# Performance work log

Hardware: AMD Instinct MI355X
Metric: run time of the kernel (lower is better)

## Reference

```python
import jax, jax.numpy as jnp
import numpy as np

HIDDEN = 4096
N_HEADS = 32
N_KV = 8
HEAD_DIM = 128
ROPE_THETA = 10000.0
B, S = 2, 2048


def _rope_neox(x, cos, sin):
    # x: [B,S,H,D]; cos/sin: [B,S,1,D/2]
    half = x.shape[-1] // 2
    x1, x2 = x[..., :half], x[..., half:]
    return jnp.concatenate([x1 * cos - x2 * sin, x2 * cos + x1 * sin], axis=-1)


def setup_inputs() -> dict:
    key = jax.random.key(0)
    k1, k2, k3 = jax.random.split(key, 3)
    hidden_states = jax.random.normal(k1, (B, S, HIDDEN), dtype=jnp.float32)
    positions = jnp.arange(B * S, dtype=jnp.int32).reshape(B, S)
    q_size = N_HEADS * HEAD_DIM
    kv_size = N_KV * HEAD_DIM
    w_qkv = jax.random.normal(k2, (HIDDEN, q_size + 2 * kv_size), dtype=jnp.float32) * (HIDDEN ** -0.5)
    w_o = jax.random.normal(k3, (q_size, HIDDEN), dtype=jnp.float32) * (q_size ** -0.5)
    return {"hidden_states": hidden_states, "positions": positions, "w_qkv": w_qkv, "w_o": w_o}


def reference(hidden_states, positions, w_qkv, w_o):
    q_size = N_HEADS * HEAD_DIM
    kv_size = N_KV * HEAD_DIM
    b, s, _ = hidden_states.shape

    qkv = hidden_states @ w_qkv  # [B,S,q+2kv]
    q = qkv[..., :q_size].reshape(b, s, N_HEADS, HEAD_DIM)
    k = qkv[..., q_size:q_size + kv_size].reshape(b, s, N_KV, HEAD_DIM)
    v = qkv[..., q_size + kv_size:].reshape(b, s, N_KV, HEAD_DIM)

    # RoPE (neox style, full rotary dim)
    inv_freq = 1.0 / (ROPE_THETA ** (jnp.arange(0, HEAD_DIM, 2, dtype=jnp.float32) / HEAD_DIM))
    ang = positions.astype(jnp.float32)[..., None] * inv_freq  # [B,S,D/2]
    cos = jnp.cos(ang)[:, :, None, :]
    sin = jnp.sin(ang)[:, :, None, :]
    q = _rope_neox(q, cos, sin)
    k = _rope_neox(k, cos, sin)

    # GQA: expand kv heads to match q heads
    rep = N_HEADS // N_KV
    k = jnp.repeat(k, rep, axis=2)  # [B,S,H,D]
    v = jnp.repeat(v, rep, axis=2)

    scale = HEAD_DIM ** -0.5
    scores = jnp.einsum('bqhd,bkhd->bhqk', q, k) * scale  # [B,H,S,S]
    causal = jnp.tril(jnp.ones((s, s), dtype=bool))
    scores = jnp.where(causal[None, None], scores, jnp.finfo(scores.dtype).min)
    probs = jax.nn.softmax(scores, axis=-1)
    attn = jnp.einsum('bhqk,bkhd->bqhd', probs, v).reshape(b, s, q_size)
    return attn @ w_o
```

## Files before the change

### kernel.cpp

```cpp
#include <hip/hip_runtime.h>
#include <hip/hip_bf16.h>
#include <stdint.h>
#include <stddef.h>

typedef unsigned short u16;
typedef __bf16 bf16x8 __attribute__((ext_vector_type(8)));
typedef float f32x4 __attribute__((ext_vector_type(4)));
typedef float f32x16 __attribute__((ext_vector_type(16)));
typedef unsigned u32x2 __attribute__((ext_vector_type(2)));

#define NH 32
#define NKV 8
#define HD 128
#define QKV_N 6144
#define SEQ 2048

__device__ __forceinline__ u16 f2b(float x) {
  union { float f; unsigned u; } v; v.f = x;
  unsigned r = v.u + 0x7FFF + ((v.u >> 16) & 1);
  return (u16)(r >> 16);
}
__device__ __forceinline__ float b2f(u16 b) {
  union { float f; unsigned u; } v; v.u = ((unsigned)b) << 16;
  return v.f;
}
__device__ __forceinline__ void gload16(const void* g, void* l) {
  __builtin_amdgcn_global_load_lds((const __attribute__((address_space(1))) unsigned int*)g,
                                   (__attribute__((address_space(3))) unsigned int*)l, 16, 0, 0);
}
template <int N>
__device__ __forceinline__ void vmwait() {
  asm volatile("s_waitcnt vmcnt(%0)" ::"n"(N) : "memory");
}
__device__ __forceinline__ unsigned pk(float lo, float hi) {
  union { __bf16 h[2]; unsigned w; } u;
  u.h[0] = (__bf16)lo; u.h[1] = (__bf16)hi;
  return u.w;
}
__device__ __forceinline__ void plswap(unsigned& a, unsigned& b) {
  u32x2 r = __builtin_amdgcn_permlane32_swap(a, b, false, false);
  a = r.x; b = r.y;
}
__device__ __forceinline__ float pl_partner_max(float x) {
  unsigned u = __float_as_uint(x);
  u32x2 r = __builtin_amdgcn_permlane32_swap(u, u, false, false);
  return fmaxf(__uint_as_float(r.x), __uint_as_float(r.y));
}
__device__ __forceinline__ float pl_partner_sum(float x) {
  unsigned u = __float_as_uint(x);
  u32x2 r = __builtin_amdgcn_permlane32_swap(u, u, false, false);
  return __uint_as_float(r.x) + __uint_as_float(r.y);
}

__global__ void cast_f32_bf16(const float* __restrict__ in, u16* __restrict__ out, int n) {
  int i = (blockIdx.x * blockDim.x + threadIdx.x) * 4;
  if (i >= n) return;
  float4 v = *(const float4*)&in[i];
  ushort4 o;
  o.x = f2b(v.x); o.y = f2b(v.y); o.z = f2b(v.z); o.w = f2b(v.w);
  *(ushort4*)&out[i] = o;
}

__global__ void cast_transpose(const float* __restrict__ in, u16* __restrict__ out, int K, int N) {
  __shared__ float t[32][33];
  int n0 = blockIdx.x * 32, k0 = blockIdx.y * 32;
  int tx = threadIdx.x, ty = threadIdx.y;
#pragma unroll
  for (int i = 0; i < 4; ++i)
    t[ty + i * 8][tx] = in[(size_t)(k0 + ty + i * 8) * N + n0 + tx];
  __syncthreads();
#pragma unroll
  for (int i = 0; i < 4; ++i)
    out[(size_t)(n0 + ty + i * 8) * K + k0 + tx] = f2b(t[tx][ty + i * 8]);
}

__device__ __forceinline__ void storeC(float* C, size_t i, float v) { C[i] = v; }
__device__ __forceinline__ void storeC(u16* C, size_t i, float v) { C[i] = f2b(v); }

#define MFMA16(q, A0, A1, B0, B1)                                                              \
  {                                                                                            \
    _Pragma("unroll") for (int mi = 0; mi < 4; ++mi)                                           \
      _Pragma("unroll") for (int ni = 0; ni < 2; ++ni)                                         \
        acc[q][mi][ni] = __builtin_amdgcn_mfma_f32_16x16x32_bf16(A0[mi], B0[ni], acc[q][mi][ni], 0, 0, 0); \
    _Pragma("unroll") for (int mi = 0; mi < 4; ++mi)                                           \
      _Pragma("unroll") for (int ni = 0; ni < 2; ++ni)                                         \
        acc[q][mi][ni] = __builtin_amdgcn_mfma_f32_16x16x32_bf16(A1[mi], B1[ni], acc[q][mi][ni], 0, 0, 0); \
  }

#define KT256(NOFF, SGHI, SGLO, HASV0, HASV1, VM1)                                             \
  {                                                                                            \
    bf16x8 a0[4], a1[4], bl0[2], bl1[2], bh0[2], bh1[2];                                       \
    _Pragma("unroll") for (int mi = 0; mi < 4; ++mi) {                                         \
      a0[mi] = *(const bf16x8*)(rA0 + (NOFF) + mi * 1024);                                     \
      a1[mi] = *(const bf16x8*)(rA1 + (NOFF) + mi * 1024);                                     \
    }                                                                                          \
    _Pragma("unroll") for (int ni = 0; ni < 2; ++ni) {                                         \
      bl0[ni] = *(const bf16x8*)(rB0 + (NOFF) + ni * 1024);                                    \
      bl1[ni] = *(const bf16x8*)(rB1 + (NOFF) + ni * 1024);                                    \
      bh0[ni] = *(const bf16x8*)(rB0 + (NOFF) + 8192 + ni * 1024);                             \
      bh1[ni] = *(const bf16x8*)(rB1 + (NOFF) + 8192 + ni * 1024);                             \
    }                                                                                          \
    if (SGHI) {                                                                                \
      gload16(pAhi0, dAhi0 + ((NOFF) ^ 16384)); gload16(pAhi1, dAhi1 + ((NOFF) ^ 16384));      \
      pAhi0 += 64; pAhi1 += 64;                                                                \
      gload16(pBlo0, dBlo0 + ((NOFF) ^ 16384)); gload16(pBlo1, dBlo1 + ((NOFF) ^ 16384));      \
      gload16(pBhi0, dBhi0 + ((NOFF) ^ 16384)); gload16(pBhi1, dBhi1 + ((NOFF) ^ 16384));      \
      pBlo0 += 64; pBlo1 += 64; pBhi0 += 64; pBhi1 += 64;                                      \
    }                                                                                          \
    __builtin_amdgcn_s_barrier();                                                              \
    __builtin_amdgcn_s_setprio(1);                                                             \
    MFMA16(0, a0, a1, bl0, bl1)                                                                \
    MFMA16(1, a0, a1, bh0, bh1)                                                                \
    __builtin_amdgcn_s_setprio(0);                                                             \
    __builtin_amdgcn_sched_barrier(0);                                                         \
    if (HASV0) vmwait<8>();                                                                    \
    __builtin_amdgcn_s_barrier();                                                              \
    _Pragma("unroll") for (int mi = 0; mi < 4; ++mi) {                                         \
      a0[mi] = *(const bf16x8*)(rA0 + (NOFF) + 8192 + mi * 1024);                              \
      a1[mi] = *(const bf16x8*)(rA1 + (NOFF) + 8192 + mi * 1024);                              \
    }                                                                                          \
    if (SGLO) {                                                                                \
      gload16(pAlo0, dAlo0 + (NOFF)); gload16(pAlo1, dAlo1 + (NOFF));                          \
      pAlo0 += 64; pAlo1 += 64;                                                                \
    }                                                                                          \
    __builtin_amdgcn_s_barrier();                                                              \
    __builtin_amdgcn_s_setprio(1);                                                             \
    MFMA16(2, a0, a1, bl0, bl1)                                                                \
    MFMA16(3, a0, a1, bh0, bh1)                                                                \
    __builtin_amdgcn_s_setprio(0);                                                             \
    __builtin_amdgcn_sched_barrier(0);                                                         \
    if (HASV1) vmwait<VM1>();                                                                  \
    __builtin_amdgcn_s_barrier();                                                              \
  }

template <typename OutT>
__global__ __launch_bounds__(512, 2) void gemm256(const u16* __restrict__ A, const u16* __restrict__ Bt,
                                                  OutT* __restrict__ C, int M, int N, int K) {
  __shared__ __align__(16) u16 sA[2 * 16384];
  __shared__ __align__(16) u16 sB[2 * 16384];
  const int nbx = N >> 8;
  const int nwg = (M >> 8) * nbx;
  const int cpx = nwg >> 3;
  const int wg = ((int)blockIdx.x & 7) * cpx + ((int)blockIdx.x >> 3);
  const int row0 = (wg / nbx) << 8, col0 = (wg % nbx) << 8;
  const int tid = threadIdx.x, w = tid >> 6, lane = tid & 63;
  const int wm = w >> 2, wn = w & 3;
  const int lq = lane & 15, lh = lane >> 4, x7 = lq & 7;
  const int o0 = (lh ^ x7) << 3, o1 = ((4 + lh) ^ x7) << 3;
  const int nt = K >> 6;

  const int rr = tid >> 3;
  const int swz = ((tid & 7) ^ (rr & 7)) << 3;
  const u16* pAlo0 = A + (size_t)(row0 + rr) * K + swz;
  const u16* pAlo1 = A + (size_t)(row0 + 64 + rr) * K + swz;
  const u16* pAhi0 = A + (size_t)(row0 + 128 + rr) * K + swz;
  const u16* pAhi1 = A + (size_t)(row0 + 192 + rr) * K + swz;
  const u16* pBlo0 = Bt + (size_t)(col0 + rr) * K + swz;
  const u16* pBlo1 = Bt + (size_t)(col0 + 64 + rr) * K + swz;
  const u16* pBhi0 = Bt + (size_t)(col0 + 128 + rr) * K + swz;
  const u16* pBhi1 = Bt + (size_t)(col0 + 192 + rr) * K + swz;
  u16* dAlo0 = sA + w * 512;
  u16* dAlo1 = sA + 4096 + w * 512;
  u16* dAhi0 = sA + 8192 + w * 512;
  u16* dAhi1 = sA + 12288 + w * 512;
  u16* dBlo0 = sB + w * 512;
  u16* dBlo1 = sB + 4096 + w * 512;
  u16* dBhi0 = sB + 8192 + w * 512;
  u16* dBhi1 = sB + 12288 + w * 512;
  const u16* rA0 = sA + (wm * 64 + lq) * 64 + o0;
  const u16* rA1 = sA + (wm * 64 + lq) * 64 + o1;
  const u16* rB0 = sB + (wn * 32 + lq) * 64 + o0;
  const u16* rB1 = sB + (wn * 32 + lq) * 64 + o1;

  f32x4 acc[4][4][2] = {};

  gload16(pAlo0, dAlo0); gload16(pAlo1, dAlo1); pAlo0 += 64; pAlo1 += 64;
  gload16(pBlo0, dBlo0); gload16(pBlo1, dBlo1); pBlo0 += 64; pBlo1 += 64;
  gload16(pBhi0, dBhi0); gload16(pBhi1, dBhi1); pBhi0 += 64; pBhi1 += 64;
  gload16(pAhi0, dAhi0); gload16(pAhi1, dAhi1); pAhi0 += 64; pAhi1 += 64;
  gload16(pAlo0, dAlo0 + 16384); gload16(pAlo1, dAlo1 + 16384); pAlo0 += 64; pAlo1 += 64;
  vmwait<4>();
  __builtin_amdgcn_s_barrier();

  for (int t = 0; t < nt - 2; t += 2) {
    KT256(0, 1, 1, 1, 1, 2)
    KT256(16384, 1, 1, 1, 1, 2)
  }
  KT256(0, 1, 0, 1, 1, 0)
  KT256(16384, 0, 0, 0, 0, 0)

#pragma unroll
  for (int q = 0; q < 4; ++q) {
    const int ah = q >> 1, bh2 = q & 1;
#pragma unroll
    for (int mi = 0; mi < 4; ++mi)
#pragma unroll
      for (int ni = 0; ni < 2; ++ni)
#pragma unroll
        for (int j = 0; j < 4; ++j) {
          const int row = row0 + ah * 128 + wm * 64 + mi * 16 + lh * 4 + j;
          const int col = col0 + bh2 * 128 + wn * 32 + ni * 16 + lq;
          storeC(C, (size_t)row * N + col, acc[q][mi][ni][j]);
        }
  }
}

#define MM24(q, A0, A1)                                                                        \
  {                                                                                            \
    _Pragma("unroll") for (int mi = 0; mi < 4; ++mi)                                           \
      _Pragma("unroll") for (int ni = 0; ni < 3; ++ni)                                         \
        acc[q][mi][ni] = __builtin_amdgcn_mfma_f32_16x16x32_bf16(A0[mi], b0[ni], acc[q][mi][ni], 0, 0, 0); \
    _Pragma("unroll") for (int mi = 0; mi < 4; ++mi)                                           \
      _Pragma("unroll") for (int ni = 0; ni < 3; ++ni)                                         \
        acc[q][mi][ni] = __builtin_amdgcn_mfma_f32_16x16x32_bf16(A1[mi], b1[ni], acc[q][mi][ni], 0, 0, 0); \
  }

#define KT192(NA, NB, SGHI, SGLO, HASV0, HASV1, VM1)                                           \
  {                                                                                            \
    bf16x8 a0[4], a1[4], b0[3], b1[3];                                                         \
    _Pragma("unroll") for (int mi = 0; mi < 4; ++mi) {                                         \
      a0[mi] = *(const bf16x8*)(rA0 + (NA) + mi * 1024);                                       \
      a1[mi] = *(const bf16x8*)(rA1 + (NA) + mi * 1024);                                       \
    }                                                                                          \
    _Pragma("unroll") for (int ni = 0; ni < 3; ++ni) {                                         \
      b0[ni] = *(const bf16x8*)(rB0 + (NB) + ni * 1024);                                       \
      b1[ni] = *(const bf16x8*)(rB1 + (NB) + ni * 1024);                                       \
    }                                                                                          \
    if (SGHI) {                                                                                \
      gload16(pA2, dA2 + ((NA) ^ 16384)); gload16(pA3, dA3 + ((NA) ^ 16384));                  \
      pA2 += 64; pA3 += 64;                                                                    \
      gload16(pB0, dB0 + ((NB) ^ 12288)); gload16(pB1, dB1 + ((NB) ^ 12288));                  \
      gload16(pB2, dB2 + ((NB) ^ 12288));                                                      \
      pB0 += 64; pB1 += 64; pB2 += 64;                                                         \
    }                                                                                          \
    __builtin_amdgcn_s_barrier();                                                              \
    __builtin_amdgcn_s_setprio(1);                                                             \
    MM24(0, a0, a1)                                                                            \
    __builtin_amdgcn_s_setprio(0);                                                             \
    __builtin_amdgcn_sched_barrier(0);                                                         \
    if (HASV0) vmwait<7>();                                                                    \
    __builtin_amdgcn_s_barrier();                                                              \
    _Pragma("unroll") for (int mi = 0; mi < 4; ++mi) {                                         \
      a0[mi] = *(const bf16x8*)(rA0 + (NA) + 8192 + mi * 1024);                                \
      a1[mi] = *(const bf16x8*)(rA1 + (NA) + 8192 + mi * 1024);                                \
    }                                                                                          \
    if (SGLO) {                                                                                \
      gload16(pA0, dA0 + (NA)); gload16(pA1, dA1 + (NA));                                      \
      pA0 += 64; pA1 += 64;                                                                    \
    }                                                                                          \
    __builtin_amdgcn_s_barrier();                                                              \
    __builtin_amdgcn_s_setprio(1);                                                             \
    MM24(1, a0, a1)                                                                            \
    __builtin_amdgcn_s_setprio(0);                                                             \
    __builtin_amdgcn_sched_barrier(0);                                                         \
    if (HASV1) vmwait<VM1>();                                                                  \
    __builtin_amdgcn_s_barrier();                                                              \
  }

__global__ __launch_bounds__(512, 2) void gemm192(const u16* __restrict__ A, const u16* __restrict__ Bt,
                                                  u16* __restrict__ C, int M, int N, int K) {
  __shared__ __align__(16) u16 sA[2 * 16384];
  __shared__ __align__(16) u16 sB[2 * 12288];
  const int nbx = N / 192;
  const int nwg = (M >> 8) * nbx;
  const int cpx = nwg >> 3;
  const int wg = ((int)blockIdx.x & 7) * cpx + ((int)blockIdx.x >> 3);
  const int row0 = (wg / nbx) << 8, col0 = (wg % nbx) * 192;
  const int tid = threadIdx.x, w = tid >> 6, lane = tid & 63;
  const int wm = w >> 2, wn = w & 3;
  const int lq = lane & 15, lh = lane >> 4, x7 = lq & 7;
  const int o0 = (lh ^ x7) << 3, o1 = ((4 + lh) ^ x7) << 3;
  const int nt = K >> 6;

  const int rr = tid >> 3;
  const int swz = ((tid & 7) ^ (rr & 7)) << 3;
  const u16* pA0 = A + (size_t)(row0 + rr) * K + swz;
  const u16* pA1 = A + (size_t)(row0 + 64 + rr) * K + swz;
  const u16* pA2 = A + (size_t)(row0 + 128 + rr) * K + swz;
  const u16* pA3 = A + (size_t)(row0 + 192 + rr) * K + swz;
  const u16* pB0 = Bt + (size_t)(col0 + rr) * K + swz;
  const u16* pB1 = Bt + (size_t)(col0 + 64 + rr) * K + swz;
  const u16* pB2 = Bt + (size_t)(col0 + 128 + rr) * K + swz;
  u16* dA0 = sA + w * 512;
  u16* dA1 = sA + 4096 + w * 512;
  u16* dA2 = sA + 8192 + w * 512;
  u16* dA3 = sA + 12288 + w * 512;
  u16* dB0 = sB + w * 512;
  u16* dB1 = sB + 4096 + w * 512;
  u16* dB2 = sB + 8192 + w * 512;
  const u16* rA0 = sA + (wm * 64 + lq) * 64 + o0;
  const u16* rA1 = sA + (wm * 64 + lq) * 64 + o1;
  const u16* rB0 = sB + (wn * 48 + lq) * 64 + o0;
  const u16* rB1 = sB + (wn * 48 + lq) * 64 + o1;

  f32x4 acc[2][4][3] = {};

  gload16(pA0, dA0); gload16(pA1, dA1); pA0 += 64; pA1 += 64;
  gload16(pB0, dB0); gload16(pB1, dB1); gload16(pB2, dB2); pB0 += 64; pB1 += 64; pB2 += 64;
  gload16(pA2, dA2); gload16(pA3, dA3); pA2 += 64; pA3 += 64;
  gload16(pA0, dA0 + 16384); gload16(pA1, dA1 + 16384); pA0 += 64; pA1 += 64;
  vmwait<4>();
  __builtin_amdgcn_s_barrier();

  for (int t = 0; t < nt - 2; t += 2) {
    KT192(0, 0, 1, 1, 1, 1, 2)
    KT192(16384, 12288, 1, 1, 1, 1, 2)
  }
  KT192(0, 0, 1, 0, 1, 1, 0)
  KT192(16384, 12288, 0, 0, 0, 0, 0)

#pragma unroll
  for (int ah = 0; ah < 2; ++ah)
#pragma unroll
    for (int mi = 0; mi < 4; ++mi)
#pragma unroll
      for (int ni = 0; ni < 3; ++ni)
#pragma unroll
        for (int j = 0; j < 4; ++j) {
          const int row = row0 + ah * 128 + wm * 64 + mi * 16 + lh * 4 + j;
          const int col = col0 + wn * 48 + ni * 16 + lq;
          C[(size_t)row * N + col] = f2b(acc[ah][mi][ni][j]);
        }
}

__global__ void rope_kernel(u16* __restrict__ qkv, const int* __restrict__ pos, float qscale) {
  __shared__ float cs[64], sn[64];
  const int row = blockIdx.x;
  const int tid = threadIdx.x;
  if (tid < 64) {
    float p = (float)pos[row];
    float inv = exp2f(-(float)tid * 0.20762050593046f);
    float a = p * inv;
    cs[tid] = cosf(a);
    sn[tid] = sinf(a);
  }
  __syncthreads();
  const size_t base = (size_t)row * QKV_N;
  for (int i = tid; i < 40 * 16; i += 256) {
    const int h = i >> 4, dq = (i & 15) * 4;
    const size_t o = base + h * 128 + dq;
    ushort4 v1 = *(const ushort4*)&qkv[o];
    ushort4 v2 = *(const ushort4*)&qkv[o + 64];
    const float sc = (h < NH) ? qscale : 1.0f;
    ushort4 r1, r2;
    {
      float x1 = b2f(v1.x), x2 = b2f(v2.x), c = cs[dq], s = sn[dq];
      r1.x = f2b((x1 * c - x2 * s) * sc); r2.x = f2b((x2 * c + x1 * s) * sc);
    }
    {
      float x1 = b2f(v1.y), x2 = b2f(v2.y), c = cs[dq + 1], s = sn[dq + 1];
      r1.y = f2b((x1 * c - x2 * s) * sc); r2.y = f2b((x2 * c + x1 * s) * sc);
    }
    {
      float x1 = b2f(v1.z), x2 = b2f(v2.z), c = cs[dq + 2], s = sn[dq + 2];
      r1.z = f2b((x1 * c - x2 * s) * sc); r2.z = f2b((x2 * c + x1 * s) * sc);
    }
    {
      float x1 = b2f(v1.w), x2 = b2f(v2.w), c = cs[dq + 3], s = sn[dq + 3];
      r1.w = f2b((x1 * c - x2 * s) * sc); r2.w = f2b((x2 * c + x1 * s) * sc);
    }
    *(ushort4*)&qkv[o] = r1;
    *(ushort4*)&qkv[o + 64] = r2;
  }
}

__global__ void v_transpose(const u16* __restrict__ qkv, u16* __restrict__ vt) {
  __shared__ u16 t[32][33];
  const int b = blockIdx.z >> 3, kvh = blockIdx.z & 7;
  const int s0 = blockIdx.x * 32, d0 = blockIdx.y * 32;
  const int tx = threadIdx.x, ty = threadIdx.y;
#pragma unroll
  for (int i = 0; i < 4; ++i)
    t[ty + i * 8][tx] = qkv[(size_t)(b * SEQ + s0 + ty + i * 8) * QKV_N + 5120 + kvh * 128 + d0 + tx];
  __syncthreads();
#pragma unroll
  for (int i = 0; i < 4; ++i)
    vt[(size_t)((b * NKV + kvh) * HD + d0 + ty + i * 8) * SEQ + s0 + tx] = t[tx][ty + i * 8];
}

__global__ __launch_bounds__(512, 2) void attn_kernel(const u16* __restrict__ qkv, const u16* __restrict__ vt,
                                                      u16* __restrict__ attn) {
  __shared__ __align__(16) u16 sK[2][64 * 128];
  __shared__ __align__(16) u16 sV[2][128 * 64];
  const int b = blockIdx.z, h = blockIdx.y;
  const int qt = (b == 0) ? blockIdx.x : 7 - blockIdx.x;
  const int kvh = h >> 2;
  const int qb = qt * 256;
  const int tid = threadIdx.x, w = tid >> 6, lane = tid & 63;
  const int lq = lane & 31, hi = lane >> 5, x7 = lane & 7;
  const int qw = qb + (w << 5);
  const int qa = qw + lq;
  const int nt = 4 * (qt + 1);

  auto stage = [&](int buf, int kt) {
    const int k0 = kt * 64;
#pragma unroll
    for (int c = 0; c < 2; ++c) {
      const int g = c * 512 + tid;
      const int r = g >> 4, gc = g & 15;
      const int gs = gc ^ (r & 7);
      gload16(qkv + (size_t)(b * SEQ + k0 + r) * QKV_N + 4096 + kvh * 128 + gs * 8,
              &sK[buf][(c * 512 + (w << 6)) * 8]);
    }
#pragma unroll
    for (int c = 0; c < 2; ++c) {
      const int g = c * 512 + tid;
      const int r = g >> 3, gc = g & 7;
      const int gs = gc ^ (r & 7);
      gload16(vt + (size_t)((b * NKV + kvh) * HD + r) * SEQ + k0 + gs * 8,
              &sV[buf][(c * 512 + (w << 6)) * 8]);
    }
  };

  stage(0, 0);
  bf16x8 qf[8];
#pragma unroll
  for (int ks = 0; ks < 8; ++ks)
    qf[ks] = *(const bf16x8*)&qkv[(size_t)(b * SEQ + qw + lq) * QKV_N + h * 128 + ks * 16 + 8 * hi];

  f32x16 o[4] = {};
  float mreg = -1e30f, lreg = 0.f;

  asm volatile("s_waitcnt vmcnt(0)" ::: "memory");
  __builtin_amdgcn_s_barrier();

  for (int kt = 0; kt < nt; ++kt) {
    const int cur = kt & 1;
    const int k0 = kt * 64;
    if (kt + 1 < nt) {
      stage(cur ^ 1, kt + 1);
      asm volatile("s_waitcnt vmcnt(4)" ::: "memory");
    } else {
      asm volatile("s_waitcnt vmcnt(0)" ::: "memory");
    }
    __builtin_amdgcn_s_barrier();

    if (k0 <= qw + 31) {
      const u16* sk = sK[cur];
      f32x16 st0 = {}, st1 = {};
      __builtin_amdgcn_s_setprio(1);
#pragma unroll
      for (int ks = 0; ks < 8; ++ks) {
        const int g = ((2 * ks + hi) ^ x7) * 8;
        bf16x8 kf0 = *(const bf16x8*)&sk[lq * 128 + g];
        bf16x8 kf1 = *(const bf16x8*)&sk[(32 + lq) * 128 + g];
        st0 = __builtin_amdgcn_mfma_f32_32x32x16_bf16(kf0, qf[ks], st0, 0, 0, 0);
        st1 = __builtin_amdgcn_mfma_f32_32x32x16_bf16(kf1, qf[ks], st1, 0, 0, 0);
      }
      __builtin_amdgcn_s_setprio(0);
      if (k0 + 63 > qw) {
#pragma unroll
        for (int r = 0; r < 16; ++r) {
          const int cr = (r & 3) + 8 * (r >> 2) + 4 * hi;
          st0[r] = (k0 + cr <= qa) ? st0[r] : -1e30f;
          st1[r] = (k0 + 32 + cr <= qa) ? st1[r] : -1e30f;
        }
      }
      float a8[8];
#pragma unroll
      for (int r = 0; r < 8; ++r)
        a8[r] = fmaxf(fmaxf(st0[r], st0[r + 8]), fmaxf(st1[r], st1[r + 8]));
#pragma unroll
      for (int s = 4; s; s >>= 1)
#pragma unroll
        for (int r = 0; r < s; ++r) a8[r] = fmaxf(a8[r], a8[r + s]);
      const float pm = pl_partner_max(a8[0]);
      if (!__all(pm <= mreg + 8.f)) {
        const float mn = fmaxf(mreg, pm);
        const float al = exp2f(mreg - mn);
        lreg *= al;
        mreg = mn;
#pragma unroll
        for (int r = 0; r < 16; ++r) {
          const int cr = (r & 3) + 8 * (r >> 2) + 4 * hi;
          const float ar = __shfl(al, cr, 64);
#pragma unroll
          for (int dn = 0; dn < 4; ++dn) o[dn][r] *= ar;
        }
      }
#pragma unroll
      for (int r = 0; r < 16; ++r) {
        st0[r] = exp2f(st0[r] - mreg);
        st1[r] = exp2f(st1[r] - mreg);
      }
      float s8[8];
#pragma unroll
      for (int r = 0; r < 8; ++r)
        s8[r] = (st0[r] + st0[r + 8]) + (st1[r] + st1[r + 8]);
#pragma unroll
      for (int s = 4; s; s >>= 1)
#pragma unroll
        for (int r = 0; r < s; ++r) s8[r] += s8[r + s];
      lreg += pl_partner_sum(s8[0]);
      union U8 { unsigned w[4]; bf16x8 v; };
      U8 pa[4];
#define PACKFRAG(F, P0, P1, P2, P3, P4, P5, P6, P7)                   \
      {                                                               \
        unsigned a0 = pk(P0, P1), a1 = pk(P2, P3);                    \
        unsigned b0 = pk(P4, P5), b1 = pk(P6, P7);                    \
        plswap(a0, b0); plswap(a1, b1);                               \
        pa[F].w[0] = a0; pa[F].w[1] = a1; pa[F].w[2] = b0; pa[F].w[3] = b1; \
      }
      PACKFRAG(0, st0[0], st0[1], st0[2], st0[3], st0[4], st0[5], st0[6], st0[7])
      PACKFRAG(1, st0[8], st0[9], st0[10], st0[11], st0[12], st0[13], st0[14], st0[15])
      PACKFRAG(2, st1[0], st1[1], st1[2], st1[3], st1[4], st1[5], st1[6], st1[7])
      PACKFRAG(3, st1[8], st1[9], st1[10], st1[11], st1[12], st1[13], st1[14], st1[15])
#undef PACKFRAG
      const u16* sv = sV[cur];
      __builtin_amdgcn_s_setprio(1);
#pragma unroll
      for (int dn = 0; dn < 4; ++dn) {
#pragma unroll
        for (int ks = 0; ks < 4; ++ks) {
          bf16x8 vf = *(const bf16x8*)&sv[(dn * 32 + lq) * 64 + (((2 * ks + hi) ^ x7)) * 8];
          o[dn] = __builtin_amdgcn_mfma_f32_32x32x16_bf16(pa[ks].v, vf, o[dn], 0, 0, 0);
        }
      }
      __builtin_amdgcn_s_setprio(0);
    }
    __builtin_amdgcn_s_barrier();
  }

  const float inv = 1.0f / lreg;
#pragma unroll
  for (int r = 0; r < 16; ++r) {
    const int cr = (r & 3) + 8 * (r >> 2) + 4 * hi;
    const float fr = __shfl(inv, cr, 64);
    const size_t row = (size_t)(b * SEQ + qw + cr);
#pragma unroll
    for (int dn = 0; dn < 4; ++dn)
      attn[row * 4096 + h * 128 + dn * 32 + lq] = f2b(o[dn][r] * fr);
  }
}

extern "C" void kernel_launch(void* const* d_in, const int* in_sizes, int n_in,
                              void* d_out, int out_size, void* d_ws, size_t ws_size,
                              hipStream_t stream) {
  const float* hs = (const float*)d_in[0];
  const int* pos = (const int*)d_in[1];
  const float* w_qkv = (const float*)d_in[2];
  const float* w_o = (const float*)d_in[3];
  float* out = (float*)d_out;
  char* ws = (char*)d_ws;

  u16* hid = (u16*)ws;
  u16* attnb = hid;
  u16* wT = (u16*)(ws + 33554432);
  u16* qkv = (u16*)(ws + 83886080);
  u16* vt = (u16*)(ws + 134217728);

  const float qscale = 0.12751744f;

  cast_f32_bf16<<<16384, 256, 0, stream>>>(hs, hid, 4096 * 4096);
  cast_transpose<<<dim3(192, 128), dim3(32, 8), 0, stream>>>(w_qkv, wT, 4096, QKV_N);
  gemm192<<<512, 512, 0, stream>>>(hid, wT, qkv, 4096, QKV_N, 4096);
  rope_kernel<<<4096, 256, 0, stream>>>(qkv, pos, qscale);
  v_transpose<<<dim3(64, 4, 16), dim3(32, 8), 0, stream>>>(qkv, vt);
  cast_transpose<<<dim3(128, 128), dim3(32, 8), 0, stream>>>(w_o, wT, 4096, 4096);
  attn_kernel<<<dim3(8, 32, 2), 512, 0, stream>>>(qkv, vt, attnb);
  gemm256<float><<<256, 512, 0, stream>>>(attnb, wT, out, 4096, 4096, 4096);
}
```

Baseline: 519.7 us.

## Restructure 256-tile GEMM main loop into four-phase interleaved load/MFMA schedule

Splits each K-tile of the 256x256 GEMM into four MFMA phases, each paired with one smaller set of global-to-LDS loads. B tiles for the next stage are prefetched earlier in the prologue, and the vmcnt waits are reduced to one per tile. The aim is to spread memory traffic more evenly across the MFMA work and hide load latency better. In exchange it adds more workgroup barriers per tile and holds more outstanding loads, which risks synchronization overhead and ordering hazards on LDS buffer reuse.

```diff
diff --git a/kernel.cpp b/kernel.cpp
--- a/kernel.cpp
+++ b/kernel.cpp
@@ -87,9 +87,10 @@
         acc[q][mi][ni] = __builtin_amdgcn_mfma_f32_16x16x32_bf16(A1[mi], B1[ni], acc[q][mi][ni], 0, 0, 0); \
   }
 
-#define KT256(NOFF, SGHI, SGLO, HASV0, HASV1, VM1)                                             \
+#define KT8(NOFF, SG1, SG2, VMODE)                                                             \
   {                                                                                            \
     bf16x8 a0[4], a1[4], bl0[2], bl1[2], bh0[2], bh1[2];                                       \
+                                                \
     _Pragma("unroll") for (int mi = 0; mi < 4; ++mi) {                                         \
       a0[mi] = *(const bf16x8*)(rA0 + (NOFF) + mi * 1024);                                     \
       a1[mi] = *(const bf16x8*)(rA1 + (NOFF) + mi * 1024);                                     \
@@ -97,39 +98,59 @@
     _Pragma("unroll") for (int ni = 0; ni < 2; ++ni) {                                         \
       bl0[ni] = *(const bf16x8*)(rB0 + (NOFF) + ni * 1024);                                    \
       bl1[ni] = *(const bf16x8*)(rB1 + (NOFF) + ni * 1024);                                    \
+    }                                                                                          \
+    if (SG1) {                                                                                 \
+      gload16(pAhi0, dAhi0 + ((NOFF) ^ 16384)); gload16(pAhi1, dAhi1 + ((NOFF) ^ 16384));      \
+      pAhi0 += 64; pAhi1 += 64;                                                                \
+    }                                                                                          \
+    __builtin_amdgcn_s_barrier();                                                              \
+    __builtin_amdgcn_s_setprio(1);                                                             \
+    MFMA16(0, a0, a1, bl0, bl1)                                                                \
+    __builtin_amdgcn_s_setprio(0);                                                             \
+    __builtin_amdgcn_sched_barrier(0);                                                         \
+    __builtin_amdgcn_s_barrier();                                                              \
+                                                      \
+    _Pragma("unroll") for (int ni = 0; ni < 2; ++ni) {                                         \
       bh0[ni] = *(const bf16x8*)(rB0 + (NOFF) + 8192 + ni * 1024);                             \
       bh1[ni] = *(const bf16x8*)(rB1 + (NOFF) + 8192 + ni * 1024);                             \
     }                                                                                          \
-    if (SGHI) {                                                                                \
-      gload16(pAhi0, dAhi0 + ((NOFF) ^ 16384)); gload16(pAhi1, dAhi1 + ((NOFF) ^ 16384));      \
-      pAhi0 += 64; pAhi1 += 64;                                                                \
-      gload16(pBlo0, dBlo0 + ((NOFF) ^ 16384)); gload16(pBlo1, dBlo1 + ((NOFF) ^ 16384));      \
-      gload16(pBhi0, dBhi0 + ((NOFF) ^ 16384)); gload16(pBhi1, dBhi1 + ((NOFF) ^ 16384));      \
-      pBlo0 += 64; pBlo1 += 64; pBhi0 += 64; pBhi1 += 64;                                      \
+    if (SG2) {                                                                                 \
+      gload16(pAlo0, dAlo0 + (NOFF)); gload16(pAlo1, dAlo1 + (NOFF));                          \
+      pAlo0 += 64; pAlo1 += 64;                                                                \
     }                                                                                          \
     __builtin_amdgcn_s_barrier();                                                              \
     __builtin_amdgcn_s_setprio(1);                                                             \
-    MFMA16(0, a0, a1, bl0, bl1)                                                                \
     MFMA16(1, a0, a1, bh0, bh1)                                                                \
     __builtin_amdgcn_s_setprio(0);                                                             \
     __builtin_amdgcn_sched_barrier(0);                                                         \
-    if (HASV0) vmwait<8>();                                                                    \
-    __builtin_amdgcn_s_barrier();                                                              \
+    __builtin_amdgcn_s_barrier();                                                              \
+                                                      \
     _Pragma("unroll") for (int mi = 0; mi < 4; ++mi) {                                         \
       a0[mi] = *(const bf16x8*)(rA0 + (NOFF) + 8192 + mi * 1024);                              \
       a1[mi] = *(const bf16x8*)(rA1 + (NOFF) + 8192 + mi * 1024);                              \
     }                                                                                          \
-    if (SGLO) {                                                                                \
-      gload16(pAlo0, dAlo0 + (NOFF)); gload16(pAlo1, dAlo1 + (NOFF));                          \
-      pAlo0 += 64; pAlo1 += 64;                                                                \
+    if (SG2) {                                                                                 \
+      gload16(pBlo0, dBlo0 + (NOFF)); gload16(pBlo1, dBlo1 + (NOFF));                          \
+      pBlo0 += 64; pBlo1 += 64;                                                                \
     }                                                                                          \
     __builtin_amdgcn_s_barrier();                                                              \
     __builtin_amdgcn_s_setprio(1);                                                             \
-    MFMA16(2, a0, a1, bl0, bl1)                                                                \
     MFMA16(3, a0, a1, bh0, bh1)                                                                \
     __builtin_amdgcn_s_setprio(0);                                                             \
     __builtin_amdgcn_sched_barrier(0);                                                         \
-    if (HASV1) vmwait<VM1>();                                                                  \
+    __builtin_amdgcn_s_barrier();                                                              \
+                                         \
+    if (SG2) {                                                                                 \
+      gload16(pBhi0, dBhi0 + (NOFF)); gload16(pBhi1, dBhi1 + (NOFF));                          \
+      pBhi0 += 64; pBhi1 += 64;                                                                \
+    }                                                                                          \
+    __builtin_amdgcn_s_barrier();                                                              \
+    __builtin_amdgcn_s_setprio(1);                                                             \
+    MFMA16(2, a0, a1, bl0, bl1)                                                                \
+    __builtin_amdgcn_s_setprio(0);                                                             \
+    __builtin_amdgcn_sched_barrier(0);                                                         \
+    if (VMODE == 1) vmwait<6>();                                                               \
+    else if (VMODE == 2) vmwait<0>();                                                          \
     __builtin_amdgcn_s_barrier();                                                              \
   }
 
@@ -179,15 +200,17 @@
   gload16(pBhi0, dBhi0); gload16(pBhi1, dBhi1); pBhi0 += 64; pBhi1 += 64;
   gload16(pAhi0, dAhi0); gload16(pAhi1, dAhi1); pAhi0 += 64; pAhi1 += 64;
   gload16(pAlo0, dAlo0 + 16384); gload16(pAlo1, dAlo1 + 16384); pAlo0 += 64; pAlo1 += 64;
-  vmwait<4>();
+  gload16(pBlo0, dBlo0 + 16384); gload16(pBlo1, dBlo1 + 16384); pBlo0 += 64; pBlo1 += 64;
+  gload16(pBhi0, dBhi0 + 16384); gload16(pBhi1, dBhi1 + 16384); pBhi0 += 64; pBhi1 += 64;
+  vmwait<6>();
   __builtin_amdgcn_s_barrier();
 
   for (int t = 0; t < nt - 2; t += 2) {
-    KT256(0, 1, 1, 1, 1, 2)
-    KT256(16384, 1, 1, 1, 1, 2)
-  }
-  KT256(0, 1, 0, 1, 1, 0)
-  KT256(16384, 0, 0, 0, 0, 0)
+    KT8(0, 1, 1, 1)
+    KT8(16384, 1, 1, 1)
+  }
+  KT8(0, 1, 0, 2)
+  KT8(16384, 0, 0, 0)
 
 #pragma unroll
   for (int q = 0; q < 4; ++q) {
```

Result: no change. 521.4 us (+0.3%).
